# Kernel optimization log

Measured on AMD Instinct MI355X. Metric: run time of the kernel, lower is better.

The kernel has to match this reference:

```python
import jax, jax.numpy as jnp
import numpy as np

R = 8          # shuffle_rate
HEADS = 4
DIM_HEAD = 64


def setup_inputs() -> dict:
    key = jax.random.key(0)
    k1, k2, k3 = jax.random.split(key, 3)
    dim = 64
    C = dim * R * R            # 4096, token channel dim after unshuffle
    inner = HEADS * DIM_HEAD   # 256
    x = jax.random.normal(k1, (8, dim, 256, 256), dtype=jnp.float32)
    W_qkv = jax.random.normal(k2, (C, 3 * inner), dtype=jnp.float32) * (C ** -0.5)
    W_out = jax.random.normal(k3, (inner, C), dtype=jnp.float32) * (inner ** -0.5)
    b_out = jnp.zeros((C,), dtype=jnp.float32)
    return {"x": x, "W_qkv": W_qkv, "W_out": W_out, "b_out": b_out}


def reference(x, W_qkv, W_out, b_out):
    scale = DIM_HEAD ** -0.5
    B, C0, H0, W0 = x.shape
    h, w = H0 // R, W0 // R
    N = h * w
    C = C0 * R * R
    # PixelUnshuffle: [B,C0,H0,W0] -> [B, C0*R*R, h, w]
    xd = x.reshape(B, C0, h, R, w, R).transpose(0, 1, 3, 5, 2, 4).reshape(B, C, h, w)
    # flatten spatial -> tokens [B, N, C]
    tokens = xd.reshape(B, C, N).transpose(0, 2, 1)
    qkv = tokens @ W_qkv                                   # [B, N, 3*inner]
    q, k, v = jnp.split(qkv, 3, axis=-1)
    def heads(t):  # [B,N,inner] -> [B,H,N,d]
        return t.reshape(B, N, HEADS, DIM_HEAD).transpose(0, 2, 1, 3)
    q, k, v = heads(q), heads(k), heads(v)
    dots = jnp.einsum('bhnd,bhmd->bhnm', q, k) * scale
    attn = jax.nn.softmax(dots, axis=-1)
    out = jnp.einsum('bhnm,bhmd->bhnd', attn, v)
    out = out.transpose(0, 2, 1, 3).reshape(B, N, HEADS * DIM_HEAD)
    y = out @ W_out + b_out                                # [B, N, C]
    y = y.transpose(0, 2, 1).reshape(B, C, h, w)
    # PixelShuffle: [B, C0*R*R, h, w] -> [B, C0, H0, W0]
    y = y.reshape(B, C0, R, R, h, w).transpose(0, 1, 4, 2, 5, 3).reshape(B, C0, H0, W0)
    return y
```

## Files before the change

kernel.cpp:

```cpp
#include <hip/hip_runtime.h>

typedef unsigned short u16;
typedef __attribute__((ext_vector_type(8))) short s16x8;
typedef __attribute__((ext_vector_type(4))) short s16x4;
typedef __attribute__((ext_vector_type(4))) float f32x4;

__device__ __forceinline__ u16 f2bf(float f) {
    unsigned int u;
    __builtin_memcpy(&u, &f, 4);
    unsigned int r = u + 0x7FFFu + ((u >> 16) & 1u);
    return (u16)(r >> 16);
}

__device__ __forceinline__ unsigned int cvt_pk_bf16(float a, float b) {
    unsigned int r;
    asm("v_cvt_pk_bf16_f32 %0, %1, %2" : "=v"(r) : "v"(a), "v"(b));
    return r;
}

__device__ __forceinline__ void gl_lds16(const u16* g, u16* l) {
    __builtin_amdgcn_global_load_lds(
        (const __attribute__((address_space(1))) unsigned int*)g,
        (__attribute__((address_space(3))) unsigned int*)l,
        16, 0, 0);
}

__global__ __launch_bounds__(256) void k_transpose(const float* __restrict__ in,
                                                   u16* __restrict__ out,
                                                   int rows, int cols) {
    __shared__ float tile[64][65];
    int bx = blockIdx.x * 64, by = blockIdx.y * 64;
    int tx = threadIdx.x & 63, ty = threadIdx.x >> 6;
    for (int i = ty; i < 64; i += 4)
        tile[i][tx] = in[(size_t)(by + i) * cols + bx + tx];
    __syncthreads();
    for (int i = ty; i < 64; i += 4)
        out[(size_t)(bx + i) * rows + by + tx] = f2bf(tile[tx][i]);
}

__global__ __launch_bounds__(256) void k_gemm_qkv(const float* __restrict__ x,
                                                  const u16* __restrict__ Bt,
                                                  float* __restrict__ P) {
    const int K = 4096;
    __shared__ u16 As[128 * 64];
    __shared__ u16 Bs[128 * 64];
    const int tid = threadIdx.x;
    const int wave = tid >> 6, lane = tid & 63;
    const int quad = lane >> 4, l15 = lane & 15;
    const int wm = wave >> 1, wn = wave & 1;

    int lin = blockIdx.x;
    int rem = (lin & 7) * 96 + (lin >> 3);
    int tn6 = rem % 6;
    int rq  = rem / 6;
    int z   = rq & 1;
    int tmi = rq >> 1;
    const int tm = tmi * 128, tn = tn6 * 128;

    const int b   = tm >> 10;
    const int yy0 = (tm & 1023) >> 5;
    const float* asrc = x + ((size_t)(b * 64 + z * 32)) * 65536 + yy0 * 2048 + tid * 8;

    u16* dstA[4];
#pragma unroll
    for (int t = 0; t < 4; ++t) {
        int row = t * 32 + (tid & 31);
        int r1  = (tid >> 5) & 7;
        int byteoff = (row * 128 + r1 * 16) ^ ((tid & 7) << 4);
        dstA[t] = (u16*)((char*)As + byteoff);
    }

    float4 va[4][2];
#pragma unroll
    for (int t = 0; t < 4; ++t) {
        const float4* sp = (const float4*)(asrc + t * 2048);
        va[t][0] = sp[0];
        va[t][1] = sp[1];
    }

    f32x4 acc[4][4] = {};

    for (int it = 0; it < 32; ++it) {
        int k0 = z * 2048 + it * 64;
        __syncthreads();
#pragma unroll
        for (int t = 0; t < 4; ++t) {
            int c = wave * 256 + t * 64 + lane;
            int row = c >> 3, kc = c & 7;
            gl_lds16(Bt + (size_t)(tn + row) * K + k0 + kc * 8,
                     Bs + (wave * 256 + t * 64) * 8);
        }
#pragma unroll
        for (int t = 0; t < 4; ++t) {
            uint4 pk;
            pk.x = cvt_pk_bf16(va[t][0].x, va[t][0].y);
            pk.y = cvt_pk_bf16(va[t][0].z, va[t][0].w);
            pk.z = cvt_pk_bf16(va[t][1].x, va[t][1].y);
            pk.w = cvt_pk_bf16(va[t][1].z, va[t][1].w);
            *(uint4*)dstA[t] = pk;
        }
        __syncthreads();
        if (it < 31) {
            asrc += 65536;
#pragma unroll
            for (int t = 0; t < 4; ++t) {
                const float4* sp = (const float4*)(asrc + t * 2048);
                va[t][0] = sp[0];
                va[t][1] = sp[1];
            }
        }
        for (int kk = 0; kk < 64; kk += 32) {
            s16x8 af[4], bf[4];
            for (int i = 0; i < 4; ++i) {
                int row = wm * 64 + i * 16 + l15;
                int byteoff = (row * 128 + kk * 2 + quad * 16) ^ ((l15 & 7) << 4);
                af[i] = *(const s16x8*)((const char*)As + byteoff);
            }
            for (int j = 0; j < 4; ++j)
                bf[j] = *(const s16x8*)(Bs + (wn * 64 + j * 16 + l15) * 64 + kk + quad * 8);
            for (int i = 0; i < 4; ++i)
                for (int j = 0; j < 4; ++j)
                    acc[i][j] = __builtin_amdgcn_mfma_f32_16x16x32_bf16(af[i], bf[j], acc[i][j], 0, 0, 0);
        }
    }

    float* Pz = P + (size_t)z * 8192 * 768;
    for (int i = 0; i < 4; ++i) {
        int mb = tm + wm * 64 + i * 16 + quad * 4;
        for (int j = 0; j < 4; ++j) {
            int col = tn + wn * 64 + j * 16 + l15;
            for (int r = 0; r < 4; ++r)
                Pz[(size_t)(mb + r) * 768 + col] = acc[i][j][r];
        }
    }
}

__global__ __launch_bounds__(256) void k_qkv_reduce(const float* __restrict__ P,
                                                    u16* __restrict__ Qo,
                                                    u16* __restrict__ Ko,
                                                    u16* __restrict__ Vt) {
    __shared__ u16 tile[64][65];
    const int tid = threadIdx.x;
    const int ct = blockIdx.x, mt = blockIdx.y;
    const int c_l = tid & 63;
    const int col = ct * 64 + c_l;
    const int mbase = mt * 64;
    const float* P1 = P + (size_t)8192 * 768;

    if (ct < 8) {
        int which = col >> 8;
        int h = (col >> 6) & 3, d = col & 63;
        u16* dst = (which == 0) ? Qo : Ko;
        for (int k = 0; k < 16; ++k) {
            int m = mbase + (tid >> 6) + k * 4;
            float v = P[(size_t)m * 768 + col] + P1[(size_t)m * 768 + col];
            int b = m >> 10, n = m & 1023;
            dst[((size_t)((b * 4 + h) * 1024 + n)) * 64 + d] = f2bf(v);
        }
    } else {
        int h = ct - 8;
        int b = mbase >> 10;
        int nbase = mbase & 1023;
        for (int k = 0; k < 16; ++k) {
            int ml = (tid >> 6) + k * 4;
            int m = mbase + ml;
            float v = P[(size_t)m * 768 + col] + P1[(size_t)m * 768 + col];
            tile[ml][c_l] = f2bf(v);
        }
        __syncthreads();
        for (int k = 0; k < 16; ++k) {
            int d = (tid >> 6) + k * 4;
            Vt[((size_t)((b * 4 + h) * 64 + d)) * 1024 + nbase + c_l] = tile[c_l][d];
        }
    }
}

__global__ __launch_bounds__(256) void k_attn(const u16* __restrict__ Qb,
                                              const u16* __restrict__ Kb,
                                              const u16* __restrict__ Vt,
                                              u16* __restrict__ aout) {
    const int bh = blockIdx.y;
    const int q0 = blockIdx.x * 64;
    const int tid = threadIdx.x;
    const int wave = tid >> 6, lane = tid & 63;
    const int quad = lane >> 4, l15 = lane & 15;
    const size_t base = (size_t)bh * 1024 * 64;
    const float scale = 0.125f;

    __shared__ u16 Ks[64 * 64];
    __shared__ u16 Vts[64 * 68];
    __shared__ u16 Ps[4][16 * 64];

    s16x8 aq0, aq1;
    {
        const u16* qp = Qb + base + (size_t)(q0 + wave * 16 + l15) * 64 + quad * 8;
        aq0 = *(const s16x8*)(qp);
        aq1 = *(const s16x8*)(qp + 32);
    }

    float m_i[4], l_i[4];
    f32x4 o[4] = {};
    for (int r = 0; r < 4; ++r) { m_i[r] = -1e30f; l_i[r] = 0.f; }

    const int vrow = tid >> 2, vpart = tid & 3;

    for (int t = 0; t < 16; ++t) {
        __syncthreads();
        for (int e = 0; e < 2; ++e) {
            int s = e * 256 + tid;
            gl_lds16(Kb + base + (size_t)t * 4096 + s * 8, Ks + s * 8);
        }
        {
            const u16* src = Vt + base + (size_t)vrow * 1024 + t * 64 + vpart * 16;
            s16x8 a = *(const s16x8*)(src);
            s16x8 b2 = *(const s16x8*)(src + 8);
            *(s16x8*)(Vts + vrow * 68 + vpart * 16) = a;
            *(s16x8*)(Vts + vrow * 68 + vpart * 16 + 8) = b2;
        }
        __syncthreads();

        f32x4 s4[4];
        for (int j = 0; j < 4; ++j) {
            const u16* kr = Ks + (j * 16 + l15) * 64 + quad * 8;
            s16x8 b0 = *(const s16x8*)(kr);
            s16x8 b1 = *(const s16x8*)(kr + 32);
            f32x4 c = {};
            c = __builtin_amdgcn_mfma_f32_16x16x32_bf16(aq0, b0, c, 0, 0, 0);
            c = __builtin_amdgcn_mfma_f32_16x16x32_bf16(aq1, b1, c, 0, 0, 0);
            s4[j] = c;
        }

        for (int r = 0; r < 4; ++r) {
            float sv0 = s4[0][r] * scale, sv1 = s4[1][r] * scale;
            float sv2 = s4[2][r] * scale, sv3 = s4[3][r] * scale;
            float mt = fmaxf(fmaxf(sv0, sv1), fmaxf(sv2, sv3));
            for (int off = 1; off < 16; off <<= 1)
                mt = fmaxf(mt, __shfl_xor(mt, off, 64));
            float mn = fmaxf(m_i[r], mt);
            float alpha = __expf(m_i[r] - mn);
            m_i[r] = mn;
            float p0 = __expf(sv0 - mn), p1 = __expf(sv1 - mn);
            float p2 = __expf(sv2 - mn), p3 = __expf(sv3 - mn);
            u16* pw = Ps[wave] + (quad * 4 + r) * 64 + l15;
            pw[0]  = f2bf(p0);
            pw[16] = f2bf(p1);
            pw[32] = f2bf(p2);
            pw[48] = f2bf(p3);
            float rs = p0 + p1 + p2 + p3;
            for (int off = 1; off < 16; off <<= 1)
                rs += __shfl_xor(rs, off, 64);
            l_i[r] = l_i[r] * alpha + rs;
            for (int dt = 0; dt < 4; ++dt) o[dt][r] *= alpha;
        }

        for (int kk = 0; kk < 64; kk += 32) {
            s16x8 pf = *(const s16x8*)(Ps[wave] + l15 * 64 + kk + quad * 8);
            for (int dt = 0; dt < 4; ++dt) {
                const u16* vr = Vts + (dt * 16 + l15) * 68 + kk + quad * 8;
                s16x4 v0 = *(const s16x4*)(vr);
                s16x4 v1 = *(const s16x4*)(vr + 4);
                s16x8 vf;
                vf[0] = v0[0]; vf[1] = v0[1]; vf[2] = v0[2]; vf[3] = v0[3];
                vf[4] = v1[0]; vf[5] = v1[1]; vf[6] = v1[2]; vf[7] = v1[3];
                o[dt] = __builtin_amdgcn_mfma_f32_16x16x32_bf16(pf, vf, o[dt], 0, 0, 0);
            }
        }
    }

    int b = bh >> 2, h = bh & 3;
    float rl[4];
    for (int r = 0; r < 4; ++r) rl[r] = 1.0f / l_i[r];
    for (int dt = 0; dt < 4; ++dt)
        for (int r = 0; r < 4; ++r) {
            int qrow = q0 + wave * 16 + quad * 4 + r;
            aout[((size_t)(b) * 1024 + qrow) * 256 + h * 64 + dt * 16 + l15] =
                f2bf(o[dt][r] * rl[r]);
        }
}

__global__ __launch_bounds__(256) void k_gemm_out(const u16* __restrict__ A,
                                                  const u16* __restrict__ Bt,
                                                  const float* __restrict__ bias,
                                                  float* __restrict__ out) {
    const int K = 256;
    __shared__ u16 As[128 * 64];
    __shared__ u16 Bs[128 * 64];
    const int tid = threadIdx.x;
    const int wave = tid >> 6, lane = tid & 63;
    const int quad = lane >> 4, l15 = lane & 15;
    const int wm = wave >> 1, wn = wave & 1;
    const int tm = blockIdx.y * 128, tn = blockIdx.x * 128;

    f32x4 acc[4][4] = {};

    for (int k0 = 0; k0 < K; k0 += 64) {
        __syncthreads();
        for (int t = 0; t < 4; ++t) {
            int c = wave * 256 + t * 64 + lane;
            int row = c >> 3, kc = c & 7;
            gl_lds16(A + (size_t)(tm + row) * K + k0 + kc * 8,
                     As + (wave * 256 + t * 64) * 8);
        }
        for (int t = 0; t < 4; ++t) {
            int c = wave * 256 + t * 64 + lane;
            int row = c >> 3, kc = c & 7;
            gl_lds16(Bt + (size_t)(tn + row) * K + k0 + kc * 8,
                     Bs + (wave * 256 + t * 64) * 8);
        }
        __syncthreads();
        for (int kk = 0; kk < 64; kk += 32) {
            s16x8 af[4], bf[4];
            for (int i = 0; i < 4; ++i)
                af[i] = *(const s16x8*)(As + (wm * 64 + i * 16 + l15) * 64 + kk + quad * 8);
            for (int j = 0; j < 4; ++j)
                bf[j] = *(const s16x8*)(Bs + (wn * 64 + j * 16 + l15) * 64 + kk + quad * 8);
            for (int i = 0; i < 4; ++i)
                for (int j = 0; j < 4; ++j)
                    acc[i][j] = __builtin_amdgcn_mfma_f32_16x16x32_bf16(af[i], bf[j], acc[i][j], 0, 0, 0);
        }
    }

    for (int i = 0; i < 4; ++i) {
        int mb = tm + wm * 64 + i * 16 + quad * 4;
        for (int j = 0; j < 4; ++j) {
            int col = tn + wn * 64 + j * 16 + l15;
            float bb = bias[col];
            int c0 = col >> 6, r1 = (col >> 3) & 7, r2 = col & 7;
            for (int r = 0; r < 4; ++r) {
                int m = mb + r;
                int b = m >> 10, n = m & 1023, yy = n >> 5, xx = n & 31;
                size_t oidx = ((size_t)((b * 64 + c0) * 256 + yy * 8 + r1)) * 256 + xx * 8 + r2;
                out[oidx] = acc[i][j][r] + bb;
            }
        }
    }
}

extern "C" void kernel_launch(void* const* d_in, const int* in_sizes, int n_in,
                              void* d_out, int out_size, void* d_ws, size_t ws_size,
                              hipStream_t stream) {
    (void)in_sizes; (void)n_in; (void)out_size; (void)ws_size;
    const float* x    = (const float*)d_in[0];
    const float* Wqkv = (const float*)d_in[1];
    const float* Wout = (const float*)d_in[2];
    const float* bout = (const float*)d_in[3];
    float* out = (float*)d_out;

    u16* ws     = (u16*)d_ws;
    u16* wqkvT  = ws;
    u16* woutT  = wqkvT + 3145728;
    u16* Qb     = woutT + 1048576;
    u16* Kb     = Qb + 2097152;
    u16* Vtb    = Kb + 2097152;
    u16* aoutb  = Vtb + 2097152;
    float* Pp   = (float*)(aoutb + 2097152);

    k_transpose<<<dim3(12, 64), 256, 0, stream>>>(Wqkv, wqkvT, 4096, 768);
    k_transpose<<<dim3(64, 4), 256, 0, stream>>>(Wout, woutT, 256, 4096);
    k_gemm_qkv<<<dim3(768, 1, 1), 256, 0, stream>>>(x, wqkvT, Pp);
    k_qkv_reduce<<<dim3(12, 128), 256, 0, stream>>>(Pp, Qb, Kb, Vtb);
    k_attn<<<dim3(16, 32), 256, 0, stream>>>(Qb, Kb, Vtb, aoutb);
    k_gemm_out<<<dim3(32, 64), 256, 0, stream>>>(aoutb, woutT, bout, out);
}
```

Baseline: 413.0 us.

## Use 256x256 QKV GEMM tiles with 512 threads and 4-way split-K

The QKV projection GEMM moves from 128x128 tiles with 256 threads and a 2-way K split to 256x256 tiles with 512 threads, 8x4 MFMA accumulators per wave, and a 4-way K split. The reduce kernel now sums four partial buffers. The larger tile raises arithmetic intensity and reuse of the x and weight loads from global memory. In exchange it writes and reads twice as much fp32 partial-sum traffic, needs more registers, and the workspace for the extra partials must be large enough.

```diff
diff --git a/kernel.cpp b/kernel.cpp
--- a/kernel.cpp
+++ b/kernel.cpp
@@ -38,95 +38,93 @@
         out[(size_t)(bx + i) * rows + by + tx] = f2bf(tile[tx][i]);
 }
 
-__global__ __launch_bounds__(256) void k_gemm_qkv(const float* __restrict__ x,
-                                                  const u16* __restrict__ Bt,
-                                                  float* __restrict__ P) {
+__global__ __launch_bounds__(512, 1) void k_gemm_qkv(const float* __restrict__ x,
+                                                     const u16* __restrict__ Bt,
+                                                     float* __restrict__ P) {
     const int K = 4096;
-    __shared__ u16 As[128 * 64];
-    __shared__ u16 Bs[128 * 64];
+    __shared__ u16 As[256 * 64];
+    __shared__ u16 Bs[256 * 64];
     const int tid = threadIdx.x;
     const int wave = tid >> 6, lane = tid & 63;
     const int quad = lane >> 4, l15 = lane & 15;
-    const int wm = wave >> 1, wn = wave & 1;
+    const int wm = wave >> 2, wn = wave & 3;
 
     int lin = blockIdx.x;
-    int rem = (lin & 7) * 96 + (lin >> 3);
-    int tn6 = rem % 6;
-    int rq  = rem / 6;
-    int z   = rq & 1;
-    int tmi = rq >> 1;
-    const int tm = tmi * 128, tn = tn6 * 128;
+    int rem = (lin & 7) * 48 + (lin >> 3);
+    int tn3 = rem % 3;
+    int q   = rem / 3;
+    int z   = q >> 5;
+    int tmi = q & 31;
+    const int tm = tmi * 256, tn = tn3 * 256;
 
     const int b   = tm >> 10;
     const int yy0 = (tm & 1023) >> 5;
-    const float* asrc = x + ((size_t)(b * 64 + z * 32)) * 65536 + yy0 * 2048 + tid * 8;
-
-    u16* dstA[4];
-#pragma unroll
-    for (int t = 0; t < 4; ++t) {
-        int row = t * 32 + (tid & 31);
-        int r1  = (tid >> 5) & 7;
-        int byteoff = (row * 128 + r1 * 16) ^ ((tid & 7) << 4);
-        dstA[t] = (u16*)((char*)As + byteoff);
-    }
-
-    float4 va[4][2];
-#pragma unroll
-    for (int t = 0; t < 4; ++t) {
-        const float4* sp = (const float4*)(asrc + t * 2048);
-        va[t][0] = sp[0];
-        va[t][1] = sp[1];
-    }
-
-    f32x4 acc[4][4] = {};
-
-    for (int it = 0; it < 32; ++it) {
-        int k0 = z * 2048 + it * 64;
-        __syncthreads();
-#pragma unroll
-        for (int t = 0; t < 4; ++t) {
-            int c = wave * 256 + t * 64 + lane;
-            int row = c >> 3, kc = c & 7;
+    const float* asrc = x + ((size_t)(b * 64 + z * 16)) * 65536
+                          + yy0 * 2048 + tid * 4;
+
+    u16* dstA[8];
+#pragma unroll
+    for (int seg = 0; seg < 8; ++seg) {
+        int xx  = (tid >> 1) & 31;
+        int row = seg * 32 + xx;
+        int k2  = wave * 16 + (tid & 1) * 8;
+        int byteoff = (row * 128 + k2) ^ ((row & 7) << 4);
+        dstA[seg] = (u16*)((char*)As + byteoff);
+    }
+
+    float4 va[8];
+#pragma unroll
+    for (int seg = 0; seg < 8; ++seg)
+        va[seg] = *(const float4*)(asrc + seg * 2048);
+
+    f32x4 acc[8][4] = {};
+
+    for (int it = 0; it < 16; ++it) {
+        int k0 = z * 1024 + it * 64;
+        __syncthreads();
+#pragma unroll
+        for (int qq = 0; qq < 4; ++qq) {
+            int chunk = qq * 512 + tid;
+            int row = chunk >> 3, kc = chunk & 7;
             gl_lds16(Bt + (size_t)(tn + row) * K + k0 + kc * 8,
-                     Bs + (wave * 256 + t * 64) * 8);
-        }
-#pragma unroll
-        for (int t = 0; t < 4; ++t) {
-            uint4 pk;
-            pk.x = cvt_pk_bf16(va[t][0].x, va[t][0].y);
-            pk.y = cvt_pk_bf16(va[t][0].z, va[t][0].w);
-            pk.z = cvt_pk_bf16(va[t][1].x, va[t][1].y);
-            pk.w = cvt_pk_bf16(va[t][1].z, va[t][1].w);
-            *(uint4*)dstA[t] = pk;
-        }
-        __syncthreads();
-        if (it < 31) {
+                     Bs + chunk * 8);
+        }
+#pragma unroll
+        for (int seg = 0; seg < 8; ++seg) {
+            uint2 pk;
+            pk.x = cvt_pk_bf16(va[seg].x, va[seg].y);
+            pk.y = cvt_pk_bf16(va[seg].z, va[seg].w);
+            *(uint2*)dstA[seg] = pk;
+        }
+        __syncthreads();
+        if (it < 15) {
             asrc += 65536;
 #pragma unroll
-            for (int t = 0; t < 4; ++t) {
-                const float4* sp = (const float4*)(asrc + t * 2048);
-                va[t][0] = sp[0];
-                va[t][1] = sp[1];
-            }
+            for (int seg = 0; seg < 8; ++seg)
+                va[seg] = *(const float4*)(asrc + seg * 2048);
         }
         for (int kk = 0; kk < 64; kk += 32) {
-            s16x8 af[4], bf[4];
-            for (int i = 0; i < 4; ++i) {
-                int row = wm * 64 + i * 16 + l15;
+            s16x8 af[8], bf[4];
+#pragma unroll
+            for (int i = 0; i < 8; ++i) {
+                int row = wm * 128 + i * 16 + l15;
                 int byteoff = (row * 128 + kk * 2 + quad * 16) ^ ((l15 & 7) << 4);
                 af[i] = *(const s16x8*)((const char*)As + byteoff);
             }
+#pragma unroll
             for (int j = 0; j < 4; ++j)
                 bf[j] = *(const s16x8*)(Bs + (wn * 64 + j * 16 + l15) * 64 + kk + quad * 8);
-            for (int i = 0; i < 4; ++i)
+#pragma unroll
+            for (int i = 0; i < 8; ++i)
+#pragma unroll
                 for (int j = 0; j < 4; ++j)
                     acc[i][j] = __builtin_amdgcn_mfma_f32_16x16x32_bf16(af[i], bf[j], acc[i][j], 0, 0, 0);
         }
     }
 
     float* Pz = P + (size_t)z * 8192 * 768;
-    for (int i = 0; i < 4; ++i) {
-        int mb = tm + wm * 64 + i * 16 + quad * 4;
+    for (int i = 0; i < 8; ++i) {
+        int mb = tm + wm * 128 + i * 16 + quad * 4;
         for (int j = 0; j < 4; ++j) {
             int col = tn + wn * 64 + j * 16 + l15;
             for (int r = 0; r < 4; ++r)
@@ -145,7 +143,10 @@
     const int c_l = tid & 63;
     const int col = ct * 64 + c_l;
     const int mbase = mt * 64;
-    const float* P1 = P + (size_t)8192 * 768;
+    const size_t NP = (size_t)8192 * 768;
+    const float* P1 = P + NP;
+    const float* P2 = P + 2 * NP;
+    const float* P3 = P + 3 * NP;
 
     if (ct < 8) {
         int which = col >> 8;
@@ -153,7 +154,8 @@
         u16* dst = (which == 0) ? Qo : Ko;
         for (int k = 0; k < 16; ++k) {
             int m = mbase + (tid >> 6) + k * 4;
-            float v = P[(size_t)m * 768 + col] + P1[(size_t)m * 768 + col];
+            size_t off = (size_t)m * 768 + col;
+            float v = P[off] + P1[off] + P2[off] + P3[off];
             int b = m >> 10, n = m & 1023;
             dst[((size_t)((b * 4 + h) * 1024 + n)) * 64 + d] = f2bf(v);
         }
@@ -164,7 +166,8 @@
         for (int k = 0; k < 16; ++k) {
             int ml = (tid >> 6) + k * 4;
             int m = mbase + ml;
-            float v = P[(size_t)m * 768 + col] + P1[(size_t)m * 768 + col];
+            size_t off = (size_t)m * 768 + col;
+            float v = P[off] + P1[off] + P2[off] + P3[off];
             tile[ml][c_l] = f2bf(v);
         }
         __syncthreads();
@@ -357,7 +360,7 @@
 
     k_transpose<<<dim3(12, 64), 256, 0, stream>>>(Wqkv, wqkvT, 4096, 768);
     k_transpose<<<dim3(64, 4), 256, 0, stream>>>(Wout, woutT, 256, 4096);
-    k_gemm_qkv<<<dim3(768, 1, 1), 256, 0, stream>>>(x, wqkvT, Pp);
+    k_gemm_qkv<<<dim3(384, 1, 1), 512, 0, stream>>>(x, wqkvT, Pp);
     k_qkv_reduce<<<dim3(12, 128), 256, 0, stream>>>(Pp, Qb, Kb, Vtb);
     k_attn<<<dim3(16, 32), 256, 0, stream>>>(Qb, Kb, Vtb, aoutb);
     k_gemm_out<<<dim3(32, 64), 256, 0, stream>>>(aoutb, woutT, bout, out);
```

Result: no change. 413.3 us (+0.1%).
